# Performance work log

Measured on AMD Instinct MI355X. Metric: run time of the kernel, lower is better.

## Reference

```python
import jax, jax.numpy as jnp
import numpy as np

H, B, T = 4, 16, 4000
E, D, A, C, K, O = 512, 512, 128, 10, 101, 512


def setup_inputs() -> dict:
    key = jax.random.key(0)
    ks = jax.random.split(key, 12)
    return {
        "enc_pad": jax.random.normal(ks[0], (B, T, E), jnp.float32),
        "enc_len": jax.random.randint(ks[1], (B,), T // 2, T + 1, jnp.int32),
        "dec_z": jax.random.normal(ks[2], (B, D), jnp.float32),
        "att_prev": jax.random.uniform(ks[3], (H, B, T), jnp.float32) / T,
        # learned parameters (per-head stacks)
        "Wenc": jax.random.normal(ks[4], (H, E, A), jnp.float32) / np.sqrt(E).astype(np.float32),
        "benc": jnp.zeros((H, A), jnp.float32),
        "Wdec": jax.random.normal(ks[5], (H, D, A), jnp.float32) / np.sqrt(D).astype(np.float32),
        "Watt": jax.random.normal(ks[6], (H, C, A), jnp.float32) / np.sqrt(C).astype(np.float32),
        "conv_w": jax.random.normal(ks[7], (H, C, K), jnp.float32) / np.sqrt(K).astype(np.float32),
        "gv": jax.random.normal(ks[8], (H, A), jnp.float32) / np.sqrt(A).astype(np.float32),
        "Wo": jax.random.normal(ks[9], (H * E, O), jnp.float32) / np.sqrt(H * E).astype(np.float32),
        "bo": jnp.zeros((O,), jnp.float32),
    }


def reference(enc_pad, enc_len, dec_z, att_prev, Wenc, benc, Wdec, Watt, conv_w, gv, Wo, bo):
    scaling = 1.0
    Hh, Bb, Tt = att_prev.shape
    Cc, Kk = conv_w.shape[1], conv_w.shape[2]
    pad_l = Kk // 2
    pad_r = Kk // 2 if Kk % 2 == 1 else Kk // 2 - 1
    # location conv: grouped 1D conv over heads. lhs [B,H,Tp], rhs [H*C,1,K]
    x = jnp.pad(att_prev.transpose(1, 0, 2), ((0, 0), (0, 0), (pad_l, pad_r)))
    rhs = conv_w.reshape(Hh * Cc, 1, Kk)
    conv = jax.lax.conv_general_dilated(
        x, rhs, window_strides=(1,), padding='VALID',
        dimension_numbers=('NCH', 'OIH', 'NCH'), feature_group_count=Hh)  # [B,H*C,T]
    conv = conv.reshape(Bb, Hh, Cc, Tt)
    att_conv = jnp.einsum('bhct,hca->bhta', conv, Watt)                    # mlp_att
    enc_proj = jnp.einsum('bte,hea->bhta', enc_pad, Wenc) + benc[None, :, None, :]  # mlp_enc
    dec_proj = jnp.einsum('bd,hda->bha', dec_z, Wdec)[:, :, None, :]       # mlp_dec
    e = jnp.einsum('bhta,ha->bht', jnp.tanh(enc_proj + dec_proj + att_conv), gv)  # gvec
    w = jax.nn.softmax(scaling * e, axis=-1)                               # [B,H,T]
    c = jnp.einsum('bht,bte->bhe', w, enc_pad).reshape(Bb, Hh * enc_pad.shape[-1])
    out = c @ Wo + bo                                                      # mlp_o
    return out, w.transpose(1, 0, 2)  # ws stacked as [H,B,T]
```

## Files before the change

### kernel.cpp

```cpp
#include <hip/hip_runtime.h>
#include <hip/hip_bf16.h>

#define H_ 4
#define B_ 16
#define T_ 4000
#define E_ 512
#define D_ 512
#define A_ 128
#define C_ 10
#define K_ 101
#define O_ 512
#define TC_ 50
#define CH_ (T_ / TC_)

typedef __attribute__((ext_vector_type(16))) float f32x16;
typedef __attribute__((ext_vector_type(8)))  short short8;

#define MFMA32(a, b, c) __builtin_amdgcn_mfma_f32_32x32x16_bf16(a, b, c, 0, 0, 0)

#define GLL16(gp, lp) __builtin_amdgcn_global_load_lds( \
    (const __attribute__((address_space(1))) unsigned int*)(gp), \
    (__attribute__((address_space(3))) unsigned int*)(lp), 16, 0, 0)

static __device__ __forceinline__ unsigned short f2bf(float x) {
  unsigned u = __float_as_uint(x);
  unsigned r = (u + 0x7FFFu + ((u >> 16) & 1u)) >> 16;
  return (unsigned short)r;
}
static __device__ __forceinline__ unsigned pk2(float a, float b) {
  return (unsigned)f2bf(a) | ((unsigned)f2bf(b) << 16);
}
static __device__ __forceinline__ unsigned cvtpk(float lo, float hi) {
  unsigned r;
  asm("v_cvt_pk_bf16_f32 %0, %1, %2" : "=v"(r) : "v"(lo), "v"(hi));
  return r;
}
static __device__ __forceinline__ uint4 packbf8(float4 f0, float4 f1) {
  uint4 u;
  u.x = cvtpk(f0.x, f0.y); u.y = cvtpk(f0.z, f0.w);
  u.z = cvtpk(f1.x, f1.y); u.w = cvtpk(f1.z, f1.w);
  return u;
}
static __device__ __forceinline__ f32x16 zero16() {
  f32x16 z;
#pragma unroll
  for (int i = 0; i < 16; ++i) z[i] = 0.f;
  return z;
}
static __device__ __forceinline__ float tanh_fast(float x) {
  return 1.0f - 2.0f / (__expf(2.0f * x) + 1.0f);
}
static __device__ __forceinline__ int swz32(int r, int ksg) {
  return (r >> 1) * 128 + (((((r & 1) << 2) | ksg) ^ ((r >> 1) & 7)) << 4);
}
static __device__ __forceinline__ int swzC(int r, int sl) {
  return r * 128 + ((sl ^ (r & 7)) << 4);
}

__global__ __launch_bounds__(256) void k_prep(const float* __restrict__ Wenc,
                                              const float* __restrict__ Watt,
                                              const float* __restrict__ dec_z,
                                              const float* __restrict__ Wdec,
                                              const float* __restrict__ benc,
                                              char* __restrict__ wbs,
                                              char* __restrict__ wattb,
                                              float* __restrict__ addv4) {
  const int bid = blockIdx.x;
  const int tid = threadIdx.x;
  if (bid < 128) {
    const int c = bid * 256 + tid;
    const int cc = c & 2047;
    const int kt = c >> 11;
    const int line = cc >> 3, sp = cc & 7;
    const int sraw = sp ^ (line & 7);
    const int n = line * 2 + (sraw >> 2);
    const int ksg = sraw & 3;
    const int h = n >> 7, a = n & 127;
    const int kb = kt * 32 + ksg * 8;
    uint4 u;
    u.x = pk2(Wenc[((size_t)h * E_ + kb + 0) * A_ + a], Wenc[((size_t)h * E_ + kb + 1) * A_ + a]);
    u.y = pk2(Wenc[((size_t)h * E_ + kb + 2) * A_ + a], Wenc[((size_t)h * E_ + kb + 3) * A_ + a]);
    u.z = pk2(Wenc[((size_t)h * E_ + kb + 4) * A_ + a], Wenc[((size_t)h * E_ + kb + 5) * A_ + a]);
    u.w = pk2(Wenc[((size_t)h * E_ + kb + 6) * A_ + a], Wenc[((size_t)h * E_ + kb + 7) * A_ + a]);
    ((uint4*)wbs)[c] = u;
  } else if (bid == 128) {
#pragma unroll
    for (int q = 0; q < 4; ++q) {
      const int cw = q * 256 + tid;
      const int h = cw >> 8, cc = cw & 255;
      const int line = cc >> 3, sp = cc & 7;
      const int sraw = sp ^ (line & 7);
      const int a = line * 4 + (sraw >> 1);
      const int s = sraw & 1;
      unsigned short v[8];
#pragma unroll
      for (int j = 0; j < 8; ++j) {
        const int k = s * 8 + j;
        v[j] = (k < C_) ? f2bf(Watt[((size_t)h * C_ + k) * A_ + a]) : (unsigned short)0;
      }
      uint4 u;
      u.x = (unsigned)v[0] | ((unsigned)v[1] << 16);
      u.y = (unsigned)v[2] | ((unsigned)v[3] << 16);
      u.z = (unsigned)v[4] | ((unsigned)v[5] << 16);
      u.w = (unsigned)v[6] | ((unsigned)v[7] << 16);
      ((uint4*)wattb)[cw] = u;
    }
  } else {
    const int idx = bid - 129;
    const int b = idx >> 3, h = (idx >> 1) & 3, ks = idx & 1;
    const int a = tid & 127, kh = tid >> 7;
    const int p = ks * 2 + kh;
    const int d0 = p * 128;
    const float* z = dec_z + (size_t)b * D_ + d0;
    const float* w = Wdec + ((size_t)h * D_ + d0) * A_ + a;
    float s = (p == 0) ? benc[h * A_ + a] : 0.f;
#pragma unroll 8
    for (int d = 0; d < 128; ++d) s += z[d] * w[(size_t)d * A_];
    addv4[(((size_t)p * B_ + b) * H_ + h) * A_ + a] = s;
  }
}

__global__ __launch_bounds__(256) void k_conv(const float* __restrict__ att_prev,
                                              const float* __restrict__ conv_w,
                                              char* __restrict__ convpad) {
  const int bh = blockIdx.x;
  const int b = bh / H_, h = bh % H_;
  const int t0 = blockIdx.y * 256;
  __shared__ float ap[256 + K_ - 1 + 3];
  __shared__ float cw[C_ * K_];
  const float* src = att_prev + ((size_t)h * B_ + b) * T_;
  for (int i = threadIdx.x; i < 256 + K_ - 1; i += 256) {
    int tt = t0 - (K_ / 2) + i;
    ap[i] = (tt >= 0 && tt < T_) ? src[tt] : 0.f;
  }
  for (int i = threadIdx.x; i < C_ * K_; i += 256) cw[i] = conv_w[(size_t)h * C_ * K_ + i];
  __syncthreads();
  const int t = t0 + threadIdx.x;
  if (t < T_) {
    float s[C_];
#pragma unroll
    for (int c = 0; c < C_; ++c) s[c] = 0.f;
    for (int k = 0; k < K_; ++k) {
      float apv = ap[threadIdx.x + k];
#pragma unroll
      for (int c = 0; c < C_; ++c) s[c] += cw[c * K_ + k] * apv;
    }
    uint4 u0, u1;
    u0.x = pk2(s[0], s[1]); u0.y = pk2(s[2], s[3]);
    u0.z = pk2(s[4], s[5]); u0.w = pk2(s[6], s[7]);
    u1.x = pk2(s[8], s[9]); u1.y = 0u; u1.z = 0u; u1.w = 0u;
    char* dst = convpad + (size_t)(b * T_ + t) * 128 + h * 32;
    *(uint4*)dst = u0;
    *(uint4*)(dst + 16) = u1;
  }
}

__global__ __launch_bounds__(512, 2) void k_fused_e_mfma(
    const float* __restrict__ enc,
    const char*  __restrict__ wbs,
    const char*  __restrict__ convpad,
    const char*  __restrict__ wattb,
    const float* __restrict__ addv4,
    const float* __restrict__ gv,
    float* __restrict__ e_out) {
  __shared__ char smem[81920];
  const int tid = threadIdx.x;
  const int wv = tid >> 6;
  const int wh = wv & 3;
  const int wm = wv >> 2;
  const int lane = tid & 63;
  const int ln31 = lane & 31;
  const int hi = lane >> 5;
  const int m0 = blockIdx.x * 128;
  const unsigned b0 = (unsigned)m0 / 4000u;
  const unsigned b1 = (unsigned)(m0 + 127) / 4000u;

  f32x16 acc[2][4];
#pragma unroll
  for (int i = 0; i < 2; ++i)
#pragma unroll
    for (int j = 0; j < 4; ++j) acc[i][j] = zero16();

  const int srow = tid >> 2, sksg = tid & 3;
  char* wrA = smem + swz32(srow, sksg);
  const float* encP = enc + (size_t)(m0 + srow) * E_ + sksg * 8;
  const char* wp = wbs + wv * 1024 + lane * 16;
  char* gllB1 = smem + 49152 + wv * 1024;
  char* gllB0 = smem + 16384 + wv * 1024;
  const int aoff = swz32(wm * 64 + ln31, hi);
  const int boff = swz32(wh * 128 + ln31, hi);
  const char* pA  = smem + aoff;
  const char* pAx = smem + (aoff ^ 32);
  const char* pB  = smem + 16384 + boff;
  const char* pBx = smem + 16384 + (boff ^ 32);

#define MSTEP(AOFF, BOFF) do {                                                  \
    { short8 a0_ = *(const short8*)(pA + (AOFF));                               \
      short8 a1_ = *(const short8*)(pA + (AOFF) + 2048);                        \
      short8 b_;                                                                \
      b_ = *(const short8*)(pB + (BOFF));                                       \
      acc[0][0] = MFMA32(a0_, b_, acc[0][0]); acc[1][0] = MFMA32(a1_, b_, acc[1][0]); \
      b_ = *(const short8*)(pB + (BOFF) + 2048);                                \
      acc[0][1] = MFMA32(a0_, b_, acc[0][1]); acc[1][1] = MFMA32(a1_, b_, acc[1][1]); \
      b_ = *(const short8*)(pB + (BOFF) + 4096);                                \
      acc[0][2] = MFMA32(a0_, b_, acc[0][2]); acc[1][2] = MFMA32(a1_, b_, acc[1][2]); \
      b_ = *(const short8*)(pB + (BOFF) + 6144);                                \
      acc[0][3] = MFMA32(a0_, b_, acc[0][3]); acc[1][3] = MFMA32(a1_, b_, acc[1][3]); } \
    { short8 a0_ = *(const short8*)(pAx + (AOFF));                              \
      short8 a1_ = *(const short8*)(pAx + (AOFF) + 2048);                       \
      short8 b_;                                                                \
      b_ = *(const short8*)(pBx + (BOFF));                                      \
      acc[0][0] = MFMA32(a0_, b_, acc[0][0]); acc[1][0] = MFMA32(a1_, b_, acc[1][0]); \
      b_ = *(const short8*)(pBx + (BOFF) + 2048);                               \
      acc[0][1] = MFMA32(a0_, b_, acc[0][1]); acc[1][1] = MFMA32(a1_, b_, acc[1][1]); \
      b_ = *(const short8*)(pBx + (BOFF) + 4096);                               \
      acc[0][2] = MFMA32(a0_, b_, acc[0][2]); acc[1][2] = MFMA32(a1_, b_, acc[1][2]); \
      b_ = *(const short8*)(pBx + (BOFF) + 6144);                               \
      acc[0][3] = MFMA32(a0_, b_, acc[0][3]); acc[1][3] = MFMA32(a1_, b_, acc[1][3]); } \
  } while (0)

#define CBAR(N) do {                                                            \
    asm volatile("s_waitcnt vmcnt(" #N ") lgkmcnt(0)" ::: "memory");            \
    __builtin_amdgcn_sched_barrier(0);                                          \
    __builtin_amdgcn_s_barrier();                                               \
  } while (0)

  float4 rA0, rA1, rB0, rB1;

#pragma unroll
  for (int it = 0; it < 4; ++it)
    GLL16(wp + it * 8192, gllB0 + it * 8192);
  __builtin_amdgcn_sched_barrier(0);
  {
    float4 t0 = ((const float4*)encP)[0];
    float4 t1 = ((const float4*)encP)[1];
    rA0 = ((const float4*)(encP + 32))[0];
    rA1 = ((const float4*)(encP + 32))[1];
    *(uint4*)wrA = packbf8(t0, t1);
  }
  encP += 64;
  wp += 32768;
  CBAR(2);

#pragma unroll 1
  for (int ktp = 0; ktp < 7; ++ktp) {
#pragma unroll
    for (int it = 0; it < 4; ++it)
      GLL16(wp + it * 8192, gllB1 + it * 8192);
    __builtin_amdgcn_sched_barrier(0);
    rB0 = ((const float4*)encP)[0];
    rB1 = ((const float4*)encP)[1];
    __builtin_amdgcn_sched_barrier(0);
    MSTEP(0, 0);
    *(uint4*)(wrA + 8192) = packbf8(rA0, rA1);
    encP += 32; wp += 32768;
    CBAR(2);
#pragma unroll
    for (int it = 0; it < 4; ++it)
      GLL16(wp + it * 8192, gllB0 + it * 8192);
    __builtin_amdgcn_sched_barrier(0);
    rA0 = ((const float4*)encP)[0];
    rA1 = ((const float4*)encP)[1];
    __builtin_amdgcn_sched_barrier(0);
    MSTEP(8192, 32768);
    *(uint4*)wrA = packbf8(rB0, rB1);
    encP += 32; wp += 32768;
    CBAR(2);
  }

#pragma unroll
  for (int it = 0; it < 4; ++it)
    GLL16(wp + it * 8192, gllB1 + it * 8192);
  __builtin_amdgcn_sched_barrier(0);
  MSTEP(0, 0);
  *(uint4*)(wrA + 8192) = packbf8(rA0, rA1);
  CBAR(0);

  {
#pragma unroll
    for (int it = 0; it < 2; ++it)
      GLL16(wattb + (size_t)it * 8192 + wv * 1024 + lane * 16, gllB0 + 16384 + it * 8192);
    __builtin_amdgcn_sched_barrier(0);
    uint4 rc0 = *(const uint4*)(convpad + (size_t)(m0 + (tid >> 3)) * 128 + (tid & 7) * 16);
    uint4 rc1 = *(const uint4*)(convpad + (size_t)(m0 + ((tid + 512) >> 3)) * 128 + (tid & 7) * 16);
    float av0s = addv4[b0 * 512 + tid]         + addv4[8192 + b0 * 512 + tid]
               + addv4[16384 + b0 * 512 + tid] + addv4[24576 + b0 * 512 + tid];
    float av1s = addv4[b1 * 512 + tid]         + addv4[8192 + b1 * 512 + tid]
               + addv4[16384 + b1 * 512 + tid] + addv4[24576 + b1 * 512 + tid];
    float gvv = gv[tid];
    __builtin_amdgcn_sched_barrier(0);
    MSTEP(8192, 32768);
    *(uint4*)(smem + 16384 + swzC(tid >> 3, tid & 7)) = rc0;
    *(uint4*)(smem + 16384 + swzC((tid + 512) >> 3, tid & 7)) = rc1;
    ((float*)smem)[tid] = av0s;
    ((float*)smem)[512 + tid] = av1s;
    ((float*)smem)[1024 + tid] = gvv;
    CBAR(0);
  }

  {
    const char* AconvL = smem + 16384;
    const char* WattL  = smem + 32768;
    const int sl = wh * 2 + hi;
    short8 ac0 = *(const short8*)(AconvL + swzC(wm * 64 + ln31, sl));
    short8 ac1 = *(const short8*)(AconvL + swzC(wm * 64 + 32 + ln31, sl));
#pragma unroll
    for (int ni = 0; ni < 4; ++ni) {
      const int a = ni * 32 + ln31;
      short8 wf = *(const short8*)(WattL + wh * 4096 + (a >> 2) * 128 +
                                   (((((a & 3) << 1) | hi) ^ ((a >> 2) & 7)) << 4));
      acc[0][ni] = MFMA32(ac0, wf, acc[0][ni]);
      acc[1][ni] = MFMA32(ac1, wf, acc[1][ni]);
    }
  }

  {
    const float* An_f = (const float*)smem;
    float av0[4], av1[4], gvr[4];
#pragma unroll
    for (int ni = 0; ni < 4; ++ni) {
      const int a = wh * 128 + ni * 32 + ln31;
      av0[ni] = An_f[a];
      av1[ni] = An_f[512 + a];
      gvr[ni] = An_f[1024 + a];
    }
#pragma unroll
    for (int mi = 0; mi < 2; ++mi) {
#pragma unroll
      for (int reg = 0; reg < 16; ++reg) {
        const int rl = wm * 64 + mi * 32 + (reg & 3) + ((reg >> 2) << 3) + (hi << 2);
        const unsigned brow = (unsigned)(m0 + rl);
        const unsigned bb = brow / 4000u;
        const unsigned tt = brow - bb * 4000u;
        const int sel = (bb != b0);
        float rs = 0.f;
#pragma unroll
        for (int ni = 0; ni < 4; ++ni) {
          float s = acc[mi][ni][reg] + (sel ? av1[ni] : av0[ni]);
          rs += gvr[ni] * tanh_fast(s);
        }
        rs += __shfl_xor(rs, 1);
        rs += __shfl_xor(rs, 2);
        rs += __shfl_xor(rs, 4);
        rs += __shfl_xor(rs, 8);
        rs += __shfl_xor(rs, 16);
        if (ln31 == 0) e_out[((size_t)bb * H_ + wh) * T_ + tt] = rs;
      }
    }
  }
#undef MSTEP
#undef CBAR
}

__global__ __launch_bounds__(256) void k_msum(const float* __restrict__ e_in,
                                              float2* __restrict__ msum) {
  const int bh = blockIdx.x;
  const float* er = e_in + (size_t)bh * T_;
  __shared__ float red[256];
  const int tid = threadIdx.x;
  float m = -1e30f;
  for (int t = tid; t < T_; t += 256) m = fmaxf(m, er[t]);
  red[tid] = m;
  __syncthreads();
  for (int s = 128; s > 0; s >>= 1) {
    if (tid < s) red[tid] = fmaxf(red[tid], red[tid + s]);
    __syncthreads();
  }
  m = red[0];
  __syncthreads();
  float sum = 0.f;
  for (int t = tid; t < T_; t += 256) sum += __expf(er[t] - m);
  red[tid] = sum;
  __syncthreads();
  for (int s = 128; s > 0; s >>= 1) {
    if (tid < s) red[tid] += red[tid + s];
    __syncthreads();
  }
  if (tid == 0) msum[bh] = make_float2(m, 1.0f / red[0]);
}

__global__ __launch_bounds__(128) void k_ctx(const float* __restrict__ enc,
                                             const float* __restrict__ e_in,
                                             const float2* __restrict__ msum,
                                             float* __restrict__ wout,
                                             float* __restrict__ partial) {
  const int b = blockIdx.x, tc = blockIdx.y;
  const int t0 = tc * CH_;
  const int tid = threadIdx.x;
  __shared__ float wls[H_ * CH_];
  for (int i = tid; i < H_ * CH_; i += 128) {
    const int h = i / CH_, tt = i - h * CH_;
    const float2 ms = msum[b * H_ + h];
    const float w = __expf(e_in[((size_t)b * H_ + h) * T_ + t0 + tt] - ms.x) * ms.y;
    wls[i] = w;
    wout[((size_t)h * B_ + b) * T_ + t0 + tt] = w;
  }
  __syncthreads();
  float4 a0 = {0,0,0,0}, a1 = {0,0,0,0}, a2 = {0,0,0,0}, a3 = {0,0,0,0};
  const float4* enc4 = (const float4*)enc;
  const size_t ebase = ((size_t)b * T_ + t0) * 128 + tid;
#pragma unroll 8
  for (int tt = 0; tt < CH_; ++tt) {
    const float4 x = enc4[ebase + (size_t)tt * 128];
    const float w0 = wls[tt], w1 = wls[CH_ + tt], w2 = wls[2 * CH_ + tt], w3 = wls[3 * CH_ + tt];
    a0.x += w0 * x.x; a0.y += w0 * x.y; a0.z += w0 * x.z; a0.w += w0 * x.w;
    a1.x += w1 * x.x; a1.y += w1 * x.y; a1.z += w1 * x.z; a1.w += w1 * x.w;
    a2.x += w2 * x.x; a2.y += w2 * x.y; a2.z += w2 * x.z; a2.w += w2 * x.w;
    a3.x += w3 * x.x; a3.y += w3 * x.y; a3.z += w3 * x.z; a3.w += w3 * x.w;
  }
  float4* p4 = (float4*)partial;
  const size_t pbase = (((size_t)tc * B_ + b) * H_) * 128 + tid;
  p4[pbase] = a0;
  p4[pbase + 128] = a1;
  p4[pbase + 256] = a2;
  p4[pbase + 384] = a3;
}

__global__ __launch_bounds__(256) void k_out_part(const float* __restrict__ partial,
                                                  const float* __restrict__ Wo,
                                                  float* __restrict__ p2) {
  const int b = blockIdx.x;
  const int o = blockIdx.y * 256 + threadIdx.x;
  const int kc = blockIdx.z;
  __shared__ float cS[256];
  const int he0 = kc * 256;
  {
    float s = 0.f;
#pragma unroll
    for (int tc = 0; tc < TC_; ++tc)
      s += partial[((size_t)tc * B_ + b) * (H_ * E_) + he0 + threadIdx.x];
    cS[threadIdx.x] = s;
  }
  __syncthreads();
  float s = 0.f;
#pragma unroll 8
  for (int i = 0; i < 256; ++i) s += cS[i] * Wo[(size_t)(he0 + i) * O_ + o];
  p2[((size_t)kc * B_ + b) * O_ + o] = s;
}

__global__ __launch_bounds__(512) void k_out_fin(const float* __restrict__ p2,
                                                 const float* __restrict__ bo,
                                                 float* __restrict__ out) {
  const int b = blockIdx.x, o = threadIdx.x;
  float s = bo[o];
#pragma unroll
  for (int kc = 0; kc < 8; ++kc) s += p2[((size_t)kc * B_ + b) * O_ + o];
  out[b * O_ + o] = s;
}

extern "C" void kernel_launch(void* const* d_in, const int* in_sizes, int n_in,
                              void* d_out, int out_size, void* d_ws, size_t ws_size,
                              hipStream_t stream) {
  (void)in_sizes; (void)n_in; (void)out_size; (void)ws_size;
  const float* enc      = (const float*)d_in[0];
  const float* dec_z    = (const float*)d_in[2];
  const float* att_prev = (const float*)d_in[3];
  const float* Wenc     = (const float*)d_in[4];
  const float* benc     = (const float*)d_in[5];
  const float* Wdec     = (const float*)d_in[6];
  const float* Watt     = (const float*)d_in[7];
  const float* conv_w   = (const float*)d_in[8];
  const float* gv       = (const float*)d_in[9];
  const float* Wo       = (const float*)d_in[10];
  const float* bo       = (const float*)d_in[11];

  float* out  = (float*)d_out;
  float* wout = out + B_ * O_;

  char* wsb = (char*)d_ws;
  float*  e_buf   = (float*)(wsb);
  char*   convpad = wsb + 1024000;
  char*   wbs     = wsb + 9216000;
  char*   wattb   = wsb + 9740288;
  float*  addv4   = (float*)(wsb + 9756672);
  float2* msum    = (float2*)(wsb + 9887744);
  float*  partial = (float*)(wsb + 9888256);
  float*  p2      = (float*)(wsb + 16441856);

  hipLaunchKernelGGL(k_prep, dim3(257), dim3(256), 0, stream,
                     Wenc, Watt, dec_z, Wdec, benc, wbs, wattb, addv4);
  hipLaunchKernelGGL(k_conv, dim3(B_ * H_, 16), dim3(256), 0, stream, att_prev, conv_w, convpad);
  hipLaunchKernelGGL(k_fused_e_mfma, dim3(500), dim3(512), 0, stream,
                     enc, wbs, convpad, wattb, addv4, gv, e_buf);
  hipLaunchKernelGGL(k_msum, dim3(B_ * H_), dim3(256), 0, stream, e_buf, msum);
  hipLaunchKernelGGL(k_ctx, dim3(B_, TC_), dim3(128), 0, stream, enc, e_buf, msum, wout, partial);
  hipLaunchKernelGGL(k_out_part, dim3(B_, O_ / 256, 8), dim3(256), 0, stream, partial, Wo, p2);
  hipLaunchKernelGGL(k_out_fin, dim3(B_), dim3(512), 0, stream, p2, bo, out);
}
```

Measured before the change: 143.4 us.

## Split fused score GEMM across two head-pair blocks to raise occupancy

The fused energy kernel now launches a second grid dimension so each block computes only two of the four heads (256 output columns instead of 512). Halving the accumulator tile frees registers and shared memory (smem drops to 48KB, launch bounds raised to 4 blocks per CU), aiming for more resident waves and better latency hiding. In exchange, the encoder tile is loaded and converted to bf16 twice, once per head pair, and an extra shared-memory reduction step combines partial per-wave sums before the write. The additive bias and gv terms are now read directly from global memory per wave instead of being staged through shared memory.

```diff
diff --git a/kernel.cpp b/kernel.cpp
--- a/kernel.cpp
+++ b/kernel.cpp
@@ -155,7 +155,7 @@
   }
 }
 
-__global__ __launch_bounds__(512, 2) void k_fused_e_mfma(
+__global__ __launch_bounds__(512, 4) void k_fused_e_mfma(
     const float* __restrict__ enc,
     const char*  __restrict__ wbs,
     const char*  __restrict__ convpad,
@@ -163,60 +163,55 @@
     const float* __restrict__ addv4,
     const float* __restrict__ gv,
     float* __restrict__ e_out) {
-  __shared__ char smem[81920];
+  __shared__ char smem[49152];
   const int tid = threadIdx.x;
   const int wv = tid >> 6;
-  const int wh = wv & 3;
   const int wm = wv >> 2;
+  const int wn = wv & 3;
   const int lane = tid & 63;
   const int ln31 = lane & 31;
   const int hi = lane >> 5;
   const int m0 = blockIdx.x * 128;
+  const int nh = blockIdx.y;
   const unsigned b0 = (unsigned)m0 / 4000u;
   const unsigned b1 = (unsigned)(m0 + 127) / 4000u;
 
-  f32x16 acc[2][4];
+  f32x16 acc[2][2];
 #pragma unroll
   for (int i = 0; i < 2; ++i)
 #pragma unroll
-    for (int j = 0; j < 4; ++j) acc[i][j] = zero16();
+    for (int j = 0; j < 2; ++j) acc[i][j] = zero16();
 
   const int srow = tid >> 2, sksg = tid & 3;
   char* wrA = smem + swz32(srow, sksg);
   const float* encP = enc + (size_t)(m0 + srow) * E_ + sksg * 8;
-  const char* wp = wbs + wv * 1024 + lane * 16;
-  char* gllB1 = smem + 49152 + wv * 1024;
-  char* gllB0 = smem + 16384 + wv * 1024;
+  const char* wp = wbs + nh * 16384 + wv * 2048 + lane * 16;
+  char* gllB0 = smem + 16384 + wv * 2048;
+  char* gllB1 = smem + 32768 + wv * 2048;
   const int aoff = swz32(wm * 64 + ln31, hi);
-  const int boff = swz32(wh * 128 + ln31, hi);
+  const int boff = swz32(wn * 64 + ln31, hi);
   const char* pA  = smem + aoff;
   const char* pAx = smem + (aoff ^ 32);
   const char* pB  = smem + 16384 + boff;
   const char* pBx = smem + 16384 + (boff ^ 32);
 
-#define MSTEP(AOFF, BOFF) do {                                                  \
-    { short8 a0_ = *(const short8*)(pA + (AOFF));                               \
-      short8 a1_ = *(const short8*)(pA + (AOFF) + 2048);                        \
-      short8 b_;                                                                \
-      b_ = *(const short8*)(pB + (BOFF));                                       \
-      acc[0][0] = MFMA32(a0_, b_, acc[0][0]); acc[1][0] = MFMA32(a1_, b_, acc[1][0]); \
-      b_ = *(const short8*)(pB + (BOFF) + 2048);                                \
-      acc[0][1] = MFMA32(a0_, b_, acc[0][1]); acc[1][1] = MFMA32(a1_, b_, acc[1][1]); \
-      b_ = *(const short8*)(pB + (BOFF) + 4096);                                \
-      acc[0][2] = MFMA32(a0_, b_, acc[0][2]); acc[1][2] = MFMA32(a1_, b_, acc[1][2]); \
-      b_ = *(const short8*)(pB + (BOFF) + 6144);                                \
-      acc[0][3] = MFMA32(a0_, b_, acc[0][3]); acc[1][3] = MFMA32(a1_, b_, acc[1][3]); } \
-    { short8 a0_ = *(const short8*)(pAx + (AOFF));                              \
-      short8 a1_ = *(const short8*)(pAx + (AOFF) + 2048);                       \
-      short8 b_;                                                                \
-      b_ = *(const short8*)(pBx + (BOFF));                                      \
-      acc[0][0] = MFMA32(a0_, b_, acc[0][0]); acc[1][0] = MFMA32(a1_, b_, acc[1][0]); \
-      b_ = *(const short8*)(pBx + (BOFF) + 2048);                               \
-      acc[0][1] = MFMA32(a0_, b_, acc[0][1]); acc[1][1] = MFMA32(a1_, b_, acc[1][1]); \
-      b_ = *(const short8*)(pBx + (BOFF) + 4096);                               \
-      acc[0][2] = MFMA32(a0_, b_, acc[0][2]); acc[1][2] = MFMA32(a1_, b_, acc[1][2]); \
-      b_ = *(const short8*)(pBx + (BOFF) + 6144);                               \
-      acc[0][3] = MFMA32(a0_, b_, acc[0][3]); acc[1][3] = MFMA32(a1_, b_, acc[1][3]); } \
+#define MSTEP(AOFF, BOFF) do {                                                   \
+    { short8 a0_ = *(const short8*)(pA  + (AOFF));                               \
+      short8 a1_ = *(const short8*)(pA  + (AOFF) + 2048);                        \
+      short8 b0_ = *(const short8*)(pB  + (BOFF));                               \
+      short8 b1_ = *(const short8*)(pB  + (BOFF) + 2048);                        \
+      acc[0][0] = MFMA32(a0_, b0_, acc[0][0]);                                   \
+      acc[1][0] = MFMA32(a1_, b0_, acc[1][0]);                                   \
+      acc[0][1] = MFMA32(a0_, b1_, acc[0][1]);                                   \
+      acc[1][1] = MFMA32(a1_, b1_, acc[1][1]); }                                 \
+    { short8 a0_ = *(const short8*)(pAx + (AOFF));                               \
+      short8 a1_ = *(const short8*)(pAx + (AOFF) + 2048);                        \
+      short8 b0_ = *(const short8*)(pBx + (BOFF));                               \
+      short8 b1_ = *(const short8*)(pBx + (BOFF) + 2048);                        \
+      acc[0][0] = MFMA32(a0_, b0_, acc[0][0]);                                   \
+      acc[1][0] = MFMA32(a1_, b0_, acc[1][0]);                                   \
+      acc[0][1] = MFMA32(a0_, b1_, acc[0][1]);                                   \
+      acc[1][1] = MFMA32(a1_, b1_, acc[1][1]); }                                 \
   } while (0)
 
 #define CBAR(N) do {                                                            \
@@ -227,9 +222,8 @@
 
   float4 rA0, rA1, rB0, rB1;
 
-#pragma unroll
-  for (int it = 0; it < 4; ++it)
-    GLL16(wp + it * 8192, gllB0 + it * 8192);
+  GLL16(wp, gllB0);
+  GLL16(wp + 1024, gllB0 + 1024);
   __builtin_amdgcn_sched_barrier(0);
   {
     float4 t0 = ((const float4*)encP)[0];
@@ -244,9 +238,8 @@
 
 #pragma unroll 1
   for (int ktp = 0; ktp < 7; ++ktp) {
-#pragma unroll
-    for (int it = 0; it < 4; ++it)
-      GLL16(wp + it * 8192, gllB1 + it * 8192);
+    GLL16(wp, gllB1);
+    GLL16(wp + 1024, gllB1 + 1024);
     __builtin_amdgcn_sched_barrier(0);
     rB0 = ((const float4*)encP)[0];
     rB1 = ((const float4*)encP)[1];
@@ -255,75 +248,68 @@
     *(uint4*)(wrA + 8192) = packbf8(rA0, rA1);
     encP += 32; wp += 32768;
     CBAR(2);
-#pragma unroll
-    for (int it = 0; it < 4; ++it)
-      GLL16(wp + it * 8192, gllB0 + it * 8192);
+    GLL16(wp, gllB0);
+    GLL16(wp + 1024, gllB0 + 1024);
     __builtin_amdgcn_sched_barrier(0);
     rA0 = ((const float4*)encP)[0];
     rA1 = ((const float4*)encP)[1];
     __builtin_amdgcn_sched_barrier(0);
-    MSTEP(8192, 32768);
+    MSTEP(8192, 16384);
     *(uint4*)wrA = packbf8(rB0, rB1);
     encP += 32; wp += 32768;
     CBAR(2);
   }
 
-#pragma unroll
-  for (int it = 0; it < 4; ++it)
-    GLL16(wp + it * 8192, gllB1 + it * 8192);
+  GLL16(wp, gllB1);
+  GLL16(wp + 1024, gllB1 + 1024);
   __builtin_amdgcn_sched_barrier(0);
   MSTEP(0, 0);
   *(uint4*)(wrA + 8192) = packbf8(rA0, rA1);
   CBAR(0);
 
   {
-#pragma unroll
-    for (int it = 0; it < 2; ++it)
-      GLL16(wattb + (size_t)it * 8192 + wv * 1024 + lane * 16, gllB0 + 16384 + it * 8192);
+    GLL16(wattb + nh * 8192 + wv * 1024 + lane * 16, smem + wv * 1024);
     __builtin_amdgcn_sched_barrier(0);
     uint4 rc0 = *(const uint4*)(convpad + (size_t)(m0 + (tid >> 3)) * 128 + (tid & 7) * 16);
     uint4 rc1 = *(const uint4*)(convpad + (size_t)(m0 + ((tid + 512) >> 3)) * 128 + (tid & 7) * 16);
-    float av0s = addv4[b0 * 512 + tid]         + addv4[8192 + b0 * 512 + tid]
-               + addv4[16384 + b0 * 512 + tid] + addv4[24576 + b0 * 512 + tid];
-    float av1s = addv4[b1 * 512 + tid]         + addv4[8192 + b1 * 512 + tid]
-               + addv4[16384 + b1 * 512 + tid] + addv4[24576 + b1 * 512 + tid];
-    float gvv = gv[tid];
-    __builtin_amdgcn_sched_barrier(0);
-    MSTEP(8192, 32768);
+    __builtin_amdgcn_sched_barrier(0);
+    MSTEP(8192, 16384);
     *(uint4*)(smem + 16384 + swzC(tid >> 3, tid & 7)) = rc0;
     *(uint4*)(smem + 16384 + swzC((tid + 512) >> 3, tid & 7)) = rc1;
-    ((float*)smem)[tid] = av0s;
-    ((float*)smem)[512 + tid] = av1s;
-    ((float*)smem)[1024 + tid] = gvv;
     CBAR(0);
   }
+
+  const int head_l = wn >> 1;
+  const int h_glob = nh * 2 + head_l;
 
   {
     const char* AconvL = smem + 16384;
-    const char* WattL  = smem + 32768;
-    const int sl = wh * 2 + hi;
+    const char* WattL  = smem + head_l * 4096;
+    const int sl = h_glob * 2 + hi;
     short8 ac0 = *(const short8*)(AconvL + swzC(wm * 64 + ln31, sl));
     short8 ac1 = *(const short8*)(AconvL + swzC(wm * 64 + 32 + ln31, sl));
 #pragma unroll
-    for (int ni = 0; ni < 4; ++ni) {
-      const int a = ni * 32 + ln31;
-      short8 wf = *(const short8*)(WattL + wh * 4096 + (a >> 2) * 128 +
-                                   (((((a & 3) << 1) | hi) ^ ((a >> 2) & 7)) << 4));
-      acc[0][ni] = MFMA32(ac0, wf, acc[0][ni]);
-      acc[1][ni] = MFMA32(ac1, wf, acc[1][ni]);
+    for (int bi = 0; bi < 2; ++bi) {
+      const int ar = (wn & 1) * 64 + bi * 32 + ln31;
+      short8 wf = *(const short8*)(WattL + (ar >> 2) * 128 +
+                                   (((((ar & 3) << 1) | hi) ^ ((ar >> 2) & 7)) << 4));
+      acc[0][bi] = MFMA32(ac0, wf, acc[0][bi]);
+      acc[1][bi] = MFMA32(ac1, wf, acc[1][bi]);
     }
   }
 
   {
-    const float* An_f = (const float*)smem;
-    float av0[4], av1[4], gvr[4];
-#pragma unroll
-    for (int ni = 0; ni < 4; ++ni) {
-      const int a = wh * 128 + ni * 32 + ln31;
-      av0[ni] = An_f[a];
-      av1[ni] = An_f[512 + a];
-      gvr[ni] = An_f[1024 + a];
+    float av0v[2], av1v[2], gvr[2];
+#pragma unroll
+    for (int bi = 0; bi < 2; ++bi) {
+      const int col = (wn & 1) * 64 + bi * 32 + ln31;
+      const int i0 = (b0 * H_ + h_glob) * A_ + col;
+      const int i1 = (b1 * H_ + h_glob) * A_ + col;
+      av0v[bi] = addv4[i0] + addv4[8192 + i0] + addv4[16384 + i0] + addv4[24576 + i0];
+      av1v[bi] = addv4[i1] + addv4[8192 + i1] + addv4[16384 + i1] + addv4[24576 + i1];
+      gvr[bi] = gv[h_glob * A_ + col];
     }
+    float* P = (float*)(smem + 8192);
 #pragma unroll
     for (int mi = 0; mi < 2; ++mi) {
 #pragma unroll
@@ -331,22 +317,33 @@
         const int rl = wm * 64 + mi * 32 + (reg & 3) + ((reg >> 2) << 3) + (hi << 2);
         const unsigned brow = (unsigned)(m0 + rl);
         const unsigned bb = brow / 4000u;
-        const unsigned tt = brow - bb * 4000u;
         const int sel = (bb != b0);
         float rs = 0.f;
 #pragma unroll
-        for (int ni = 0; ni < 4; ++ni) {
-          float s = acc[mi][ni][reg] + (sel ? av1[ni] : av0[ni]);
-          rs += gvr[ni] * tanh_fast(s);
+        for (int bi = 0; bi < 2; ++bi) {
+          float s = acc[mi][bi][reg] + (sel ? av1v[bi] : av0v[bi]);
+          rs += gvr[bi] * tanh_fast(s);
         }
         rs += __shfl_xor(rs, 1);
         rs += __shfl_xor(rs, 2);
         rs += __shfl_xor(rs, 4);
         rs += __shfl_xor(rs, 8);
         rs += __shfl_xor(rs, 16);
-        if (ln31 == 0) e_out[((size_t)bb * H_ + wh) * T_ + tt] = rs;
+        if (ln31 == 0) P[wv * 64 + (rl & 63)] = rs;
       }
     }
+  }
+  __syncthreads();
+
+  if (tid < 256) {
+    const float* P = (const float*)(smem + 8192);
+    const int hl = tid >> 7, rl = tid & 127;
+    const int wmf = rl >> 6, r64 = rl & 63;
+    const float ev = P[(wmf * 4 + hl * 2) * 64 + r64] + P[(wmf * 4 + hl * 2 + 1) * 64 + r64];
+    const unsigned brow = (unsigned)(m0 + rl);
+    const unsigned bb = brow / 4000u;
+    const unsigned tt = brow - bb * 4000u;
+    e_out[((size_t)bb * H_ + nh * 2 + hl) * T_ + tt] = ev;
   }
 #undef MSTEP
 #undef CBAR
@@ -480,7 +477,7 @@
   hipLaunchKernelGGL(k_prep, dim3(257), dim3(256), 0, stream,
                      Wenc, Watt, dec_z, Wdec, benc, wbs, wattb, addv4);
   hipLaunchKernelGGL(k_conv, dim3(B_ * H_, 16), dim3(256), 0, stream, att_prev, conv_w, convpad);
-  hipLaunchKernelGGL(k_fused_e_mfma, dim3(500), dim3(512), 0, stream,
+  hipLaunchKernelGGL(k_fused_e_mfma, dim3(500, 2), dim3(512), 0, stream,
                      enc, wbs, convpad, wattb, addv4, gv, e_buf);
   hipLaunchKernelGGL(k_msum, dim3(B_ * H_), dim3(256), 0, stream, e_buf, msum);
   hipLaunchKernelGGL(k_ctx, dim3(B_, TC_), dim3(128), 0, stream, enc, e_buf, msum, wout, partial);
```

Result: slower. 147.0 us (+2.5%).
